# Performance work log

Hardware: AMD Instinct MI355X
Metric: run time of the kernel (lower is better)

Reference implementation:

```python
import jax, jax.numpy as jnp
import numpy as np

N = 100000
E = 1600000
IN_FEATS = 128
HID = 128


def _xavier(key, shape):
    fan_in, fan_out = shape[0], shape[1]
    limit = float(np.sqrt(6.0 / (fan_in + fan_out)))
    return jax.random.uniform(key, shape, jnp.float32, -limit, limit)


def setup_inputs() -> dict:
    key = jax.random.key(0)
    ks = jax.random.split(key, 10)
    x = jax.random.normal(ks[0], (N, IN_FEATS), jnp.float32)
    edge_index = jax.random.randint(ks[1], (2, E), 0, N, jnp.int64)
    inp = {"x": x, "edge_index": edge_index}
    # GCNConv weights (stored as [in, out] so h = x @ W)
    inp["W1"] = _xavier(ks[2], (IN_FEATS, HID)); inp["b1"] = jnp.zeros((HID,), jnp.float32)
    inp["W2"] = _xavier(ks[3], (HID, HID));      inp["b2"] = jnp.zeros((HID,), jnp.float32)
    inp["W3"] = _xavier(ks[4], (HID, HID));      inp["b3"] = jnp.zeros((HID,), jnp.float32)
    # position head: Linear(HID,HID) -> ReLU -> Linear(HID,2)
    inp["Wp1"] = _xavier(ks[5], (HID, HID)); inp["bp1"] = jnp.zeros((HID,), jnp.float32)
    inp["Wp2"] = _xavier(ks[6], (HID, 2));   inp["bp2"] = jnp.zeros((2,), jnp.float32)
    # time head: Linear(HID,HID//2) -> ReLU -> Linear(HID//2,1)
    inp["Wt1"] = _xavier(ks[7], (HID, HID // 2)); inp["bt1"] = jnp.zeros((HID // 2,), jnp.float32)
    inp["Wt2"] = _xavier(ks[8], (HID // 2, 1));   inp["bt2"] = jnp.zeros((1,), jnp.float32)
    return inp


def _gcn_conv(x, src, dst, norm, W, b):
    # PyG GCNConv: out = D^{-1/2} (A + I) D^{-1/2} (x W) + b
    h = x @ W                                  # [N, out]
    msg = h[src] * norm[:, None]               # gather over edges (+ self-loops)
    agg = jax.ops.segment_sum(msg, dst, num_segments=N)  # scatter-add to dst
    return agg + b


def reference(x, edge_index, W1, b1, W2, b2, W3, b3, Wp1, bp1, Wp2, bp2, Wt1, bt1, Wt2, bt2):
    src, dst = edge_index[0], edge_index[1]
    # add self-loops once (shared across the 3 conv layers)
    loop = jnp.arange(N, dtype=edge_index.dtype)
    src_a = jnp.concatenate([src, loop])
    dst_a = jnp.concatenate([dst, loop])
    # symmetric normalization: deg computed on dst (in-degree incl. self-loop)
    deg = jax.ops.segment_sum(jnp.ones_like(dst_a, dtype=x.dtype), dst_a, num_segments=N)
    dinv = jnp.where(deg > 0, jax.lax.rsqrt(deg), 0.0)
    norm = dinv[src_a] * dinv[dst_a]           # [E + N]

    h = jax.nn.relu(_gcn_conv(x, src_a, dst_a, norm, W1, b1))
    h = jax.nn.relu(_gcn_conv(h, src_a, dst_a, norm, W2, b2))
    h = jax.nn.relu(_gcn_conv(h, src_a, dst_a, norm, W3, b3))

    pos = jax.nn.relu(h @ Wp1 + bp1) @ Wp2 + bp2     # [N, 2]
    time = jax.nn.relu(h @ Wt1 + bt1) @ Wt2 + bt2    # [N, 1]
    return jnp.concatenate([pos, time], axis=1)      # [N, 3]
```

## Files before the change

### kernel.cpp

```cpp
#include <hip/hip_runtime.h>

typedef __bf16 bf16x8 __attribute__((ext_vector_type(8)));
typedef unsigned short u16x8 __attribute__((ext_vector_type(8)));
typedef float f32x4 __attribute__((ext_vector_type(4)));

union BU {
    u16x8 u;
    bf16x8 b;
};

static __device__ __forceinline__ float b2f(unsigned short u) {
    return __uint_as_float(((unsigned)u) << 16);
}
static __device__ __forceinline__ unsigned short f2b(float f) {
    unsigned u = __float_as_uint(f);
    unsigned r = (u + 0x7FFF + ((u >> 16) & 1)) >> 16;
    return (unsigned short)r;
}

__global__ __launch_bounds__(256) void wsplit_kernel(
    const float* __restrict__ W1, const float* __restrict__ W2, const float* __restrict__ W3,
    const float* __restrict__ Wp1, const float* __restrict__ Wt1,
    unsigned short* __restrict__ W1hi, unsigned short* __restrict__ W1lo,
    unsigned short* __restrict__ W2hi, unsigned short* __restrict__ W2lo,
    unsigned short* __restrict__ W3hi, unsigned short* __restrict__ W3lo,
    unsigned short* __restrict__ Wchi, unsigned short* __restrict__ Wclo,
    const float* __restrict__ bp1, const float* __restrict__ bt1, float* __restrict__ bcat) {
    int b = blockIdx.x;
    int tid = threadIdx.x;
    if (b < 288) {
        const float* W;
        unsigned short *Whi, *Wlo;
        int lb, ncshift, total;
        if (b < 64)       { W = W1;  Whi = W1hi; Wlo = W1lo; lb = b;       ncshift = 7; total = 16384; }
        else if (b < 128) { W = W2;  Whi = W2hi; Wlo = W2lo; lb = b - 64;  ncshift = 7; total = 16384; }
        else if (b < 192) { W = W3;  Whi = W3hi; Wlo = W3lo; lb = b - 128; ncshift = 7; total = 16384; }
        else if (b < 256) { W = Wp1; Whi = Wchi; Wlo = Wclo; lb = b - 192; ncshift = 7; total = 16384; }
        else              { W = Wt1; Whi = Wchi + 128 * 128; Wlo = Wclo + 128 * 128; lb = b - 256; ncshift = 6; total = 8192; }
        int idx = lb * 256 + tid;
        if (idx < total) {
            int k = idx >> ncshift;
            int n = idx - (k << ncshift);
            float a = W[idx];
            unsigned short hb = f2b(a);
            Whi[(n << 7) + k] = hb;
            Wlo[(n << 7) + k] = f2b(a - b2f(hb));
        }
        return;
    }
    if (tid < 128) bcat[tid] = bp1[tid];
    else if (tid < 192) bcat[tid] = bt1[tid - 128];
}

static __device__ __forceinline__ void split8(const float4 a01, const float4 a23,
                                              bf16x8& hi, bf16x8& lo) {
    float a[8] = {a01.x, a01.y, a01.z, a01.w, a23.x, a23.y, a23.z, a23.w};
    BU h, l;
#pragma unroll
    for (int j = 0; j < 8; ++j) {
        unsigned short hb = f2b(a[j]);
        h.u[j] = hb;
        l.u[j] = f2b(a[j] - b2f(hb));
    }
    hi = h.b;
    lo = l.b;
}

template <int NT>
static __device__ __forceinline__ void gemm_acc_f32(const float* __restrict__ A,
                                                    const unsigned short* __restrict__ Whi,
                                                    const unsigned short* __restrict__ Wlo,
                                                    int arow, int m16, int quad, f32x4* acc) {
    const float* Arow = A + (size_t)arow * 128 + quad * 8;
#pragma unroll
    for (int kb = 0; kb < 4; ++kb) {
        float4 a01 = *reinterpret_cast<const float4*>(Arow + kb * 32);
        float4 a23 = *reinterpret_cast<const float4*>(Arow + kb * 32 + 4);
        bf16x8 ahi, alo;
        split8(a01, a23, ahi, alo);
#pragma unroll
        for (int t = 0; t < NT; ++t) {
            size_t woff = (size_t)(t * 16 + m16) * 128 + quad * 8 + kb * 32;
            BU bh, bl;
            bh.u = *reinterpret_cast<const u16x8*>(Whi + woff);
            bl.u = *reinterpret_cast<const u16x8*>(Wlo + woff);
            acc[t] = __builtin_amdgcn_mfma_f32_16x16x32_bf16(ahi, bh.b, acc[t], 0, 0, 0);
            acc[t] = __builtin_amdgcn_mfma_f32_16x16x32_bf16(ahi, bl.b, acc[t], 0, 0, 0);
            acc[t] = __builtin_amdgcn_mfma_f32_16x16x32_bf16(alo, bh.b, acc[t], 0, 0, 0);
        }
    }
}

template <int NT>
static __device__ __forceinline__ void gemm_acc(const unsigned short* __restrict__ A,
                                                const unsigned short* __restrict__ Whi,
                                                const unsigned short* __restrict__ Wlo,
                                                int arow, int m16, int quad, f32x4* acc) {
    const unsigned short* Arow = A + (size_t)arow * 128 + quad * 8;
#pragma unroll
    for (int kb = 0; kb < 4; ++kb) {
        BU a;
        a.u = *reinterpret_cast<const u16x8*>(Arow + kb * 32);
#pragma unroll
        for (int t = 0; t < NT; ++t) {
            size_t woff = (size_t)(t * 16 + m16) * 128 + quad * 8 + kb * 32;
            BU bh, bl;
            bh.u = *reinterpret_cast<const u16x8*>(Whi + woff);
            bl.u = *reinterpret_cast<const u16x8*>(Wlo + woff);
            acc[t] = __builtin_amdgcn_mfma_f32_16x16x32_bf16(a.b, bh.b, acc[t], 0, 0, 0);
            acc[t] = __builtin_amdgcn_mfma_f32_16x16x32_bf16(a.b, bl.b, acc[t], 0, 0, 0);
        }
    }
}

template <int NT>
static __device__ __forceinline__ void gemm_store_plain(unsigned short* __restrict__ C,
                                                        int row_base, int m16, int quad,
                                                        f32x4* acc, int nrows) {
#pragma unroll
    for (int t = 0; t < NT; ++t) {
#pragma unroll
        for (int r = 0; r < 4; ++r) {
            int row = row_base + quad * 4 + r;
            if (row < nrows)
                C[(size_t)row * (NT * 16) + t * 16 + m16] = f2b(acc[t][r]);
        }
    }
}

template <int NT>
static __device__ __forceinline__ void gemm_store_scaled(const int* __restrict__ deg,
                                                         unsigned short* __restrict__ C,
                                                         int row_base, int m16, int quad,
                                                         f32x4* acc, int nrows) {
#pragma unroll
    for (int t = 0; t < NT; ++t) {
#pragma unroll
        for (int r = 0; r < 4; ++r) {
            int row = row_base + quad * 4 + r;
            if (row < nrows) {
                float d = rsqrtf((float)deg[row] + 1.0f);
                C[(size_t)row * (NT * 16) + t * 16 + m16] = f2b(acc[t][r] * d);
            }
        }
    }
}

__global__ __launch_bounds__(256) void fg2_kernel(const float* __restrict__ A,
                                                  const unsigned short* __restrict__ Whi,
                                                  const unsigned short* __restrict__ Wlo,
                                                  unsigned short* __restrict__ C, int nrows,
                                                  int fbn,
                                                  const int* __restrict__ ei,
                                                  int* __restrict__ deg,
                                                  int* __restrict__ slots, int E) {
    const int bid = blockIdx.x;
    const int tid = threadIdx.x;
    const int trip = bid / 3, r = bid % 3;
    if (r == 1 && trip < fbn) {
        int base = (trip * 256 + tid) * 8;
        int dsts[8], srcs[8], ps[8];
#pragma unroll
        for (int k = 0; k < 8; ++k) {
            int e = base + k;
            dsts[k] = (e < E) ? ei[E + e] : -1;
            srcs[k] = (e < E) ? ei[e] : 0;
        }
#pragma unroll
        for (int k = 0; k < 8; ++k)
            if (dsts[k] >= 0) ps[k] = atomicAdd(&deg[dsts[k]], 1);
#pragma unroll
        for (int k = 0; k < 8; ++k)
            if (dsts[k] >= 0 && ps[k] < 64)
                __builtin_nontemporal_store(srcs[k], &slots[(size_t)dsts[k] * 64 + ps[k]]);
    } else {
        int gid = bid - min(trip, fbn) - ((r > 1 && trip < fbn) ? 1 : 0);
        const int wave = tid >> 6, lane = tid & 63;
        const int m16 = lane & 15, quad = lane >> 4;
        const int row_base = gid * 64 + wave * 16;
        int arow = row_base + m16;
        if (arow >= nrows) arow = nrows - 1;
        f32x4 acc[8] = {};
        gemm_acc_f32<8>(A, Whi, Wlo, arow, m16, quad, acc);
        gemm_store_plain<8>(C, row_base, m16, quad, acc, nrows);
    }
}

__global__ __launch_bounds__(256) void scale_kernel(unsigned short* __restrict__ hs,
                                                    const int* __restrict__ deg, int n) {
    int idx = blockIdx.x * 256 + threadIdx.x;
    int node = idx >> 5;
    if (node >= n) return;
    int f = (idx & 31) * 4;
    float d = rsqrtf((float)deg[node] + 1.0f);
    ushort4 v = *reinterpret_cast<const ushort4*>(hs + (size_t)node * 128 + f);
    ushort4 o;
    o.x = f2b(b2f(v.x) * d);
    o.y = f2b(b2f(v.y) * d);
    o.z = f2b(b2f(v.z) * d);
    o.w = f2b(b2f(v.w) * d);
    *reinterpret_cast<ushort4*>(hs + (size_t)node * 128 + f) = o;
}

template <int NT>
__global__ __launch_bounds__(256) void gemm_kernel(const unsigned short* __restrict__ A,
                                                   const unsigned short* __restrict__ Whi,
                                                   const unsigned short* __restrict__ Wlo,
                                                   const int* __restrict__ deg,
                                                   unsigned short* __restrict__ C, int nrows) {
    const int tid = threadIdx.x;
    const int wave = tid >> 6, lane = tid & 63;
    const int m16 = lane & 15, quad = lane >> 4;
    const int row_base = blockIdx.x * 64 + wave * 16;
    int arow = row_base + m16;
    if (arow >= nrows) arow = nrows - 1;
    f32x4 acc[NT] = {};
    gemm_acc<NT>(A, Whi, Wlo, arow, m16, quad, acc);
    gemm_store_scaled<NT>(deg, C, row_base, m16, quad, acc, nrows);
}

__global__ __launch_bounds__(256) void pull_kernel(const unsigned short* __restrict__ hs,
                                                   const int* __restrict__ slots,
                                                   const int* __restrict__ deg,
                                                   const float* __restrict__ bias,
                                                   unsigned short* __restrict__ out, int n) {
    const int tid = threadIdx.x;
    const int wave = tid >> 6, lane = tid & 63;
    const int slot = lane >> 4, chunk = lane & 15;
    const int node = blockIdx.x * 4 + wave;
    if (node >= n) return;
    const int dg = deg[node];
    const float d = rsqrtf((float)dg + 1.0f);
    const int m = min(dg, 64);

    BU sv;
    sv.u = *reinterpret_cast<const u16x8*>(hs + (size_t)node * 128 + chunk * 8);
    int myidx = slots[(size_t)node * 64 + lane];

    float acc[8] = {};
    const int rounds = (m + 3) >> 2;
    int r = 0;
    for (; r + 4 <= rounds; r += 4) {
        int e0 = r * 4 + slot, e1 = e0 + 4, e2 = e0 + 8, e3 = e0 + 12;
        int s0 = __shfl(myidx, e0), s1 = __shfl(myidx, e1);
        int s2 = __shfl(myidx, e2), s3 = __shfl(myidx, e3);
        s0 = (unsigned)s0 < (unsigned)n ? s0 : 0;
        s1 = (unsigned)s1 < (unsigned)n ? s1 : 0;
        s2 = (unsigned)s2 < (unsigned)n ? s2 : 0;
        s3 = (unsigned)s3 < (unsigned)n ? s3 : 0;
        bool ok0 = e0 < m, ok1 = e1 < m, ok2 = e2 < m, ok3 = e3 < m;
        BU h0, h1, h2, h3;
        if (ok0) h0.u = *reinterpret_cast<const u16x8*>(hs + (size_t)s0 * 128 + chunk * 8);
        if (ok1) h1.u = *reinterpret_cast<const u16x8*>(hs + (size_t)s1 * 128 + chunk * 8);
        if (ok2) h2.u = *reinterpret_cast<const u16x8*>(hs + (size_t)s2 * 128 + chunk * 8);
        if (ok3) h3.u = *reinterpret_cast<const u16x8*>(hs + (size_t)s3 * 128 + chunk * 8);
        if (ok0) {
#pragma unroll
            for (int j = 0; j < 8; ++j) acc[j] += b2f(h0.u[j]);
        }
        if (ok1) {
#pragma unroll
            for (int j = 0; j < 8; ++j) acc[j] += b2f(h1.u[j]);
        }
        if (ok2) {
#pragma unroll
            for (int j = 0; j < 8; ++j) acc[j] += b2f(h2.u[j]);
        }
        if (ok3) {
#pragma unroll
            for (int j = 0; j < 8; ++j) acc[j] += b2f(h3.u[j]);
        }
    }
    for (; r < rounds; ++r) {
        int e0 = r * 4 + slot;
        int s0 = __shfl(myidx, e0);
        s0 = (unsigned)s0 < (unsigned)n ? s0 : 0;
        if (e0 < m) {
            BU h0;
            h0.u = *reinterpret_cast<const u16x8*>(hs + (size_t)s0 * 128 + chunk * 8);
#pragma unroll
            for (int j = 0; j < 8; ++j) acc[j] += b2f(h0.u[j]);
        }
    }
#pragma unroll
    for (int j = 0; j < 8; ++j) {
        acc[j] += __shfl_xor(acc[j], 16);
        acc[j] += __shfl_xor(acc[j], 32);
    }
    if (slot == 0) {
        BU o;
#pragma unroll
        for (int j = 0; j < 8; ++j)
            o.u[j] = f2b(fmaxf((acc[j] + b2f(sv.u[j])) * d + bias[chunk * 8 + j], 0.f));
        *reinterpret_cast<u16x8*>(out + (size_t)node * 128 + chunk * 8) = o.u;
    }
}

__global__ __launch_bounds__(256) void gemmh_kernel(const unsigned short* __restrict__ A,
                                                    const unsigned short* __restrict__ Whi,
                                                    const unsigned short* __restrict__ Wlo,
                                                    const float* __restrict__ bcat,
                                                    const float* __restrict__ Wp2,
                                                    const float* __restrict__ bp2,
                                                    const float* __restrict__ Wt2,
                                                    const float* __restrict__ bt2,
                                                    float* __restrict__ out, int nrows) {
    const int tid = threadIdx.x;
    const int wave = tid >> 6, lane = tid & 63;
    const int m16 = lane & 15, quad = lane >> 4;
    const int row_base = blockIdx.x * 64 + wave * 16;
    int arow = row_base + m16;
    if (arow >= nrows) arow = nrows - 1;
    f32x4 acc[12] = {};
    gemm_acc<12>(A, Whi, Wlo, arow, m16, quad, acc);
#pragma unroll
    for (int r = 0; r < 4; ++r) {
        int row = row_base + quad * 4 + r;
        float p0 = 0.f, p1 = 0.f, tt = 0.f;
#pragma unroll
        for (int t = 0; t < 12; ++t) {
            int c = t * 16 + m16;
            float v = fmaxf(acc[t][r] + bcat[c], 0.f);
            if (t < 8) {
                p0 += v * Wp2[c * 2 + 0];
                p1 += v * Wp2[c * 2 + 1];
            } else {
                tt += v * Wt2[c - 128];
            }
        }
#pragma unroll
        for (int mask = 1; mask < 16; mask <<= 1) {
            p0 += __shfl_xor(p0, mask);
            p1 += __shfl_xor(p1, mask);
            tt += __shfl_xor(tt, mask);
        }
        if (m16 == 0 && row < nrows) {
            out[(size_t)row * 3 + 0] = p0 + bp2[0];
            out[(size_t)row * 3 + 1] = p1 + bp2[1];
            out[(size_t)row * 3 + 2] = tt + bt2[0];
        }
    }
}

extern "C" void kernel_launch(void* const* d_in, const int* in_sizes, int n_in,
                              void* d_out, int out_size, void* d_ws, size_t ws_size,
                              hipStream_t stream) {
    const int N = in_sizes[0] / 128;
    const int E = in_sizes[1] / 2;

    const float* x   = (const float*)d_in[0];
    const int* ei    = (const int*)d_in[1];
    const float* W1  = (const float*)d_in[2];
    const float* b1  = (const float*)d_in[3];
    const float* W2  = (const float*)d_in[4];
    const float* b2  = (const float*)d_in[5];
    const float* W3  = (const float*)d_in[6];
    const float* b3  = (const float*)d_in[7];
    const float* Wp1 = (const float*)d_in[8];
    const float* bp1 = (const float*)d_in[9];
    const float* Wp2 = (const float*)d_in[10];
    const float* bp2 = (const float*)d_in[11];
    const float* Wt1 = (const float*)d_in[12];
    const float* bt1 = (const float*)d_in[13];
    const float* Wt2 = (const float*)d_in[14];
    const float* bt2 = (const float*)d_in[15];
    float* out = (float*)d_out;

    char* ws = (char*)d_ws;
    size_t off = 0;
    auto alloc = [&](size_t bytes) {
        void* p = ws + off;
        off += (bytes + 255) & ~(size_t)255;
        return p;
    };
    int* deg        = (int*)alloc((size_t)N * 4);
    int* slots      = (int*)alloc((size_t)N * 64 * 4);
    unsigned short* W1hi = (unsigned short*)alloc(16384 * 2);
    unsigned short* W1lo = (unsigned short*)alloc(16384 * 2);
    unsigned short* W2hi = (unsigned short*)alloc(16384 * 2);
    unsigned short* W2lo = (unsigned short*)alloc(16384 * 2);
    unsigned short* W3hi = (unsigned short*)alloc(16384 * 2);
    unsigned short* W3lo = (unsigned short*)alloc(16384 * 2);
    unsigned short* Wchi = (unsigned short*)alloc(192 * 128 * 2);
    unsigned short* Wclo = (unsigned short*)alloc(192 * 128 * 2);
    float* bcat          = (float*)alloc(192 * 4);
    unsigned short* hs   = (unsigned short*)alloc((size_t)N * 128 * 2);
    unsigned short* hb   = (unsigned short*)alloc((size_t)N * 128 * 2);

    hipMemsetAsync(deg, 0, (size_t)N * 4, stream);

    wsplit_kernel<<<289, 256, 0, stream>>>(W1, W2, W3, Wp1, Wt1,
                                           W1hi, W1lo, W2hi, W2lo, W3hi, W3lo,
                                           Wchi, Wclo, bp1, bt1, bcat);

    const int gb = (N + 63) / 64;
    const int fbn = ((E + 7) / 8 + 255) / 256;
    const int pull_blocks = (N + 3) / 4;

    fg2_kernel<<<gb + fbn, 256, 0, stream>>>(x, W1hi, W1lo, hs, N, fbn, ei, deg, slots, E);
    scale_kernel<<<(N * 32 + 255) / 256, 256, 0, stream>>>(hs, deg, N);

    pull_kernel<<<pull_blocks, 256, 0, stream>>>(hs, slots, deg, b1, hb, N);
    gemm_kernel<8><<<gb, 256, 0, stream>>>(hb, W2hi, W2lo, deg, hs, N);
    pull_kernel<<<pull_blocks, 256, 0, stream>>>(hs, slots, deg, b2, hb, N);
    gemm_kernel<8><<<gb, 256, 0, stream>>>(hb, W3hi, W3lo, deg, hs, N);
    pull_kernel<<<pull_blocks, 256, 0, stream>>>(hs, slots, deg, b3, hb, N);

    gemmh_kernel<<<gb, 256, 0, stream>>>(hb, Wchi, Wclo, bcat, Wp2, bp2, Wt2, bt2, out, N);
}
```

Before: 631.9 us.

## Fuse neighbor aggregation with following GEMM through LDS staging

Merges each pull (gather-aggregate) kernel with the next layer's GEMM (or the output heads GEMM). Each wave aggregates 16 nodes sequentially into a padded LDS tile and then runs the MFMA GEMM from LDS. This removes the round trip of the intermediate bf16 activation buffer through global memory and several kernel launches. In exchange, each wave now walks its 16 nodes one after another, so there is less parallelism and fewer blocks in flight for latency hiding during the gather.

```diff
diff --git a/kernel.cpp b/kernel.cpp
--- a/kernel.cpp
+++ b/kernel.cpp
@@ -17,6 +17,8 @@
     unsigned r = (u + 0x7FFF + ((u >> 16) & 1)) >> 16;
     return (unsigned short)r;
 }
+
+#define LROW 136
 
 __global__ __launch_bounds__(256) void wsplit_kernel(
     const float* __restrict__ W1, const float* __restrict__ W2, const float* __restrict__ W3,
@@ -92,11 +94,11 @@
 }
 
 template <int NT>
-static __device__ __forceinline__ void gemm_acc(const unsigned short* __restrict__ A,
-                                                const unsigned short* __restrict__ Whi,
-                                                const unsigned short* __restrict__ Wlo,
-                                                int arow, int m16, int quad, f32x4* acc) {
-    const unsigned short* Arow = A + (size_t)arow * 128 + quad * 8;
+static __device__ __forceinline__ void gemm_acc_lds(const unsigned short* __restrict__ Alds,
+                                                    const unsigned short* __restrict__ Whi,
+                                                    const unsigned short* __restrict__ Wlo,
+                                                    int m16, int quad, f32x4* acc) {
+    const unsigned short* Arow = Alds + m16 * LROW + quad * 8;
 #pragma unroll
     for (int kb = 0; kb < 4; ++kb) {
         BU a;
@@ -202,37 +204,12 @@
     *reinterpret_cast<ushort4*>(hs + (size_t)node * 128 + f) = o;
 }
 
-template <int NT>
-__global__ __launch_bounds__(256) void gemm_kernel(const unsigned short* __restrict__ A,
-                                                   const unsigned short* __restrict__ Whi,
-                                                   const unsigned short* __restrict__ Wlo,
-                                                   const int* __restrict__ deg,
-                                                   unsigned short* __restrict__ C, int nrows) {
-    const int tid = threadIdx.x;
-    const int wave = tid >> 6, lane = tid & 63;
-    const int m16 = lane & 15, quad = lane >> 4;
-    const int row_base = blockIdx.x * 64 + wave * 16;
-    int arow = row_base + m16;
-    if (arow >= nrows) arow = nrows - 1;
-    f32x4 acc[NT] = {};
-    gemm_acc<NT>(A, Whi, Wlo, arow, m16, quad, acc);
-    gemm_store_scaled<NT>(deg, C, row_base, m16, quad, acc, nrows);
-}
-
-__global__ __launch_bounds__(256) void pull_kernel(const unsigned short* __restrict__ hs,
-                                                   const int* __restrict__ slots,
-                                                   const int* __restrict__ deg,
-                                                   const float* __restrict__ bias,
-                                                   unsigned short* __restrict__ out, int n) {
-    const int tid = threadIdx.x;
-    const int wave = tid >> 6, lane = tid & 63;
-    const int slot = lane >> 4, chunk = lane & 15;
-    const int node = blockIdx.x * 4 + wave;
-    if (node >= n) return;
-    const int dg = deg[node];
-    const float d = rsqrtf((float)dg + 1.0f);
+static __device__ __forceinline__ void pull_node(const unsigned short* __restrict__ hs,
+                                                 const int* __restrict__ slots,
+                                                 int node, int dg, float d, const float* bi,
+                                                 unsigned short* __restrict__ ldsrow,
+                                                 int slot, int chunk, int lane, int n) {
     const int m = min(dg, 64);
-
     BU sv;
     sv.u = *reinterpret_cast<const u16x8*>(hs + (size_t)node * 128 + chunk * 8);
     int myidx = slots[(size_t)node * 64 + lane];
@@ -291,28 +268,83 @@
         BU o;
 #pragma unroll
         for (int j = 0; j < 8; ++j)
-            o.u[j] = f2b(fmaxf((acc[j] + b2f(sv.u[j])) * d + bias[chunk * 8 + j], 0.f));
-        *reinterpret_cast<u16x8*>(out + (size_t)node * 128 + chunk * 8) = o.u;
-    }
-}
-
-__global__ __launch_bounds__(256) void gemmh_kernel(const unsigned short* __restrict__ A,
-                                                    const unsigned short* __restrict__ Whi,
-                                                    const unsigned short* __restrict__ Wlo,
-                                                    const float* __restrict__ bcat,
-                                                    const float* __restrict__ Wp2,
-                                                    const float* __restrict__ bp2,
-                                                    const float* __restrict__ Wt2,
-                                                    const float* __restrict__ bt2,
-                                                    float* __restrict__ out, int nrows) {
+            o.u[j] = f2b(fmaxf((acc[j] + b2f(sv.u[j])) * d + bi[j], 0.f));
+        *reinterpret_cast<u16x8*>(ldsrow + chunk * 8) = o.u;
+    }
+}
+
+__global__ __launch_bounds__(256) void pg_kernel(const unsigned short* __restrict__ hs_in,
+                                                 const int* __restrict__ slots,
+                                                 const int* __restrict__ deg,
+                                                 const float* __restrict__ bias,
+                                                 const unsigned short* __restrict__ Whi,
+                                                 const unsigned short* __restrict__ Wlo,
+                                                 unsigned short* __restrict__ hs_out, int n) {
+    __shared__ unsigned short lds[4 * 16 * LROW];
     const int tid = threadIdx.x;
     const int wave = tid >> 6, lane = tid & 63;
+    const int slot = lane >> 4, chunk = lane & 15;
+    const int row_base = blockIdx.x * 64 + wave * 16;
+    unsigned short* wl = lds + wave * 16 * LROW;
+
+    float bi[8];
+#pragma unroll
+    for (int j = 0; j < 8; ++j) bi[j] = bias[chunk * 8 + j];
+
+    for (int i = 0; i < 16; ++i) {
+        int node = row_base + i;
+        if (node < n) {
+            int dg = deg[node];
+            float d = rsqrtf((float)dg + 1.0f);
+            pull_node(hs_in, slots, node, dg, d, bi, wl + i * LROW, slot, chunk, lane, n);
+        } else if (slot == 0) {
+            u16x8 z = {};
+            *reinterpret_cast<u16x8*>(wl + i * LROW + chunk * 8) = z;
+        }
+    }
     const int m16 = lane & 15, quad = lane >> 4;
+    f32x4 acc[8] = {};
+    gemm_acc_lds<8>(wl, Whi, Wlo, m16, quad, acc);
+    gemm_store_scaled<8>(deg, hs_out, row_base, m16, quad, acc, n);
+}
+
+__global__ __launch_bounds__(256) void pgh_kernel(const unsigned short* __restrict__ hs_in,
+                                                  const int* __restrict__ slots,
+                                                  const int* __restrict__ deg,
+                                                  const float* __restrict__ bias,
+                                                  const unsigned short* __restrict__ Whi,
+                                                  const unsigned short* __restrict__ Wlo,
+                                                  const float* __restrict__ bcat,
+                                                  const float* __restrict__ Wp2,
+                                                  const float* __restrict__ bp2,
+                                                  const float* __restrict__ Wt2,
+                                                  const float* __restrict__ bt2,
+                                                  float* __restrict__ out, int n) {
+    __shared__ unsigned short lds[4 * 16 * LROW];
+    const int tid = threadIdx.x;
+    const int wave = tid >> 6, lane = tid & 63;
+    const int slot = lane >> 4, chunk = lane & 15;
     const int row_base = blockIdx.x * 64 + wave * 16;
-    int arow = row_base + m16;
-    if (arow >= nrows) arow = nrows - 1;
+    unsigned short* wl = lds + wave * 16 * LROW;
+
+    float bi[8];
+#pragma unroll
+    for (int j = 0; j < 8; ++j) bi[j] = bias[chunk * 8 + j];
+
+    for (int i = 0; i < 16; ++i) {
+        int node = row_base + i;
+        if (node < n) {
+            int dg = deg[node];
+            float d = rsqrtf((float)dg + 1.0f);
+            pull_node(hs_in, slots, node, dg, d, bi, wl + i * LROW, slot, chunk, lane, n);
+        } else if (slot == 0) {
+            u16x8 z = {};
+            *reinterpret_cast<u16x8*>(wl + i * LROW + chunk * 8) = z;
+        }
+    }
+    const int m16 = lane & 15, quad = lane >> 4;
     f32x4 acc[12] = {};
-    gemm_acc<12>(A, Whi, Wlo, arow, m16, quad, acc);
+    gemm_acc_lds<12>(wl, Whi, Wlo, m16, quad, acc);
 #pragma unroll
     for (int r = 0; r < 4; ++r) {
         int row = row_base + quad * 4 + r;
@@ -334,7 +366,7 @@
             p1 += __shfl_xor(p1, mask);
             tt += __shfl_xor(tt, mask);
         }
-        if (m16 == 0 && row < nrows) {
+        if (m16 == 0 && row < n) {
             out[(size_t)row * 3 + 0] = p0 + bp2[0];
             out[(size_t)row * 3 + 1] = p1 + bp2[1];
             out[(size_t)row * 3 + 2] = tt + bt2[0];
@@ -384,8 +416,8 @@
     unsigned short* Wchi = (unsigned short*)alloc(192 * 128 * 2);
     unsigned short* Wclo = (unsigned short*)alloc(192 * 128 * 2);
     float* bcat          = (float*)alloc(192 * 4);
-    unsigned short* hs   = (unsigned short*)alloc((size_t)N * 128 * 2);
-    unsigned short* hb   = (unsigned short*)alloc((size_t)N * 128 * 2);
+    unsigned short* hsA  = (unsigned short*)alloc((size_t)N * 128 * 2);
+    unsigned short* hsB  = (unsigned short*)alloc((size_t)N * 128 * 2);
 
     hipMemsetAsync(deg, 0, (size_t)N * 4, stream);
 
@@ -395,16 +427,12 @@
 
     const int gb = (N + 63) / 64;
     const int fbn = ((E + 7) / 8 + 255) / 256;
-    const int pull_blocks = (N + 3) / 4;
-
-    fg2_kernel<<<gb + fbn, 256, 0, stream>>>(x, W1hi, W1lo, hs, N, fbn, ei, deg, slots, E);
-    scale_kernel<<<(N * 32 + 255) / 256, 256, 0, stream>>>(hs, deg, N);
-
-    pull_kernel<<<pull_blocks, 256, 0, stream>>>(hs, slots, deg, b1, hb, N);
-    gemm_kernel<8><<<gb, 256, 0, stream>>>(hb, W2hi, W2lo, deg, hs, N);
-    pull_kernel<<<pull_blocks, 256, 0, stream>>>(hs, slots, deg, b2, hb, N);
-    gemm_kernel<8><<<gb, 256, 0, stream>>>(hb, W3hi, W3lo, deg, hs, N);
-    pull_kernel<<<pull_blocks, 256, 0, stream>>>(hs, slots, deg, b3, hb, N);
-
-    gemmh_kernel<<<gb, 256, 0, stream>>>(hb, Wchi, Wclo, bcat, Wp2, bp2, Wt2, bt2, out, N);
-}
+
+    fg2_kernel<<<gb + fbn, 256, 0, stream>>>(x, W1hi, W1lo, hsA, N, fbn, ei, deg, slots, E);
+    scale_kernel<<<(N * 32 + 255) / 256, 256, 0, stream>>>(hsA, deg, N);
+
+    pg_kernel<<<gb, 256, 0, stream>>>(hsA, slots, deg, b1, W2hi, W2lo, hsB, N);
+    pg_kernel<<<gb, 256, 0, stream>>>(hsB, slots, deg, b2, W3hi, W3lo, hsA, N);
+    pgh_kernel<<<gb, 256, 0, stream>>>(hsA, slots, deg, b3, Wchi, Wclo, bcat,
+                                       Wp2, bp2, Wt2, bt2, out, N);
+}
```

Result: slower. 673.7 us (+6.6%).

## Store node features in 16-column feature slices for cache-local neighbor gathers

Applied to the files above, without the earlier changes.

Node feature buffers move from row-major [N,128] to eight feature slices of [N,16]. The pull kernel now handles one slice per block, so each node's gathered working set is 3.2 MB per slice, which may stay cache-resident across neighbors. Each wave now covers up to 64 neighbors with one 16-byte load per lane, where before it looped in rounds. The GEMM, scale and head kernels are updated for the sliced layout. In exchange, the pull kernel launches eight times as many blocks, re-reads slot lists and degrees once per slice, and needs more shuffle reductions.

```diff
diff --git a/kernel.cpp b/kernel.cpp
--- a/kernel.cpp
+++ b/kernel.cpp
@@ -17,6 +17,7 @@
     unsigned r = (u + 0x7FFF + ((u >> 16) & 1)) >> 16;
     return (unsigned short)r;
 }
+
 
 __global__ __launch_bounds__(256) void wsplit_kernel(
     const float* __restrict__ W1, const float* __restrict__ W2, const float* __restrict__ W3,
@@ -92,18 +93,19 @@
 }
 
 template <int NT>
-static __device__ __forceinline__ void gemm_acc(const unsigned short* __restrict__ A,
-                                                const unsigned short* __restrict__ Whi,
-                                                const unsigned short* __restrict__ Wlo,
-                                                int arow, int m16, int quad, f32x4* acc) {
-    const unsigned short* Arow = A + (size_t)arow * 128 + quad * 8;
+static __device__ __forceinline__ void gemm_acc_sliced(const unsigned short* __restrict__ A,
+                                                       const unsigned short* __restrict__ Whi,
+                                                       const unsigned short* __restrict__ Wlo,
+                                                       int arow, int m16, int quad, f32x4* acc,
+                                                       int Nn) {
 #pragma unroll
     for (int kb = 0; kb < 4; ++kb) {
+        int f0 = kb * 32 + quad * 8;
         BU a;
-        a.u = *reinterpret_cast<const u16x8*>(Arow + kb * 32);
+        a.u = *reinterpret_cast<const u16x8*>(A + ((size_t)(f0 >> 4) * Nn + arow) * 16 + (f0 & 15));
 #pragma unroll
         for (int t = 0; t < NT; ++t) {
-            size_t woff = (size_t)(t * 16 + m16) * 128 + quad * 8 + kb * 32;
+            size_t woff = (size_t)(t * 16 + m16) * 128 + f0;
             BU bh, bl;
             bh.u = *reinterpret_cast<const u16x8*>(Whi + woff);
             bl.u = *reinterpret_cast<const u16x8*>(Wlo + woff);
@@ -114,25 +116,25 @@
 }
 
 template <int NT>
-static __device__ __forceinline__ void gemm_store_plain(unsigned short* __restrict__ C,
-                                                        int row_base, int m16, int quad,
-                                                        f32x4* acc, int nrows) {
+static __device__ __forceinline__ void gemm_store_plain_sliced(unsigned short* __restrict__ C,
+                                                               int row_base, int m16, int quad,
+                                                               f32x4* acc, int nrows) {
 #pragma unroll
     for (int t = 0; t < NT; ++t) {
 #pragma unroll
         for (int r = 0; r < 4; ++r) {
             int row = row_base + quad * 4 + r;
             if (row < nrows)
-                C[(size_t)row * (NT * 16) + t * 16 + m16] = f2b(acc[t][r]);
-        }
-    }
-}
-
-template <int NT>
-static __device__ __forceinline__ void gemm_store_scaled(const int* __restrict__ deg,
-                                                         unsigned short* __restrict__ C,
-                                                         int row_base, int m16, int quad,
-                                                         f32x4* acc, int nrows) {
+                C[((size_t)t * nrows + row) * 16 + m16] = f2b(acc[t][r]);
+        }
+    }
+}
+
+template <int NT>
+static __device__ __forceinline__ void gemm_store_scaled_sliced(const int* __restrict__ deg,
+                                                                unsigned short* __restrict__ C,
+                                                                int row_base, int m16, int quad,
+                                                                f32x4* acc, int nrows) {
 #pragma unroll
     for (int t = 0; t < NT; ++t) {
 #pragma unroll
@@ -140,7 +142,7 @@
             int row = row_base + quad * 4 + r;
             if (row < nrows) {
                 float d = rsqrtf((float)deg[row] + 1.0f);
-                C[(size_t)row * (NT * 16) + t * 16 + m16] = f2b(acc[t][r] * d);
+                C[((size_t)t * nrows + row) * 16 + m16] = f2b(acc[t][r] * d);
             }
         }
     }
@@ -182,24 +184,24 @@
         if (arow >= nrows) arow = nrows - 1;
         f32x4 acc[8] = {};
         gemm_acc_f32<8>(A, Whi, Wlo, arow, m16, quad, acc);
-        gemm_store_plain<8>(C, row_base, m16, quad, acc, nrows);
+        gemm_store_plain_sliced<8>(C, row_base, m16, quad, acc, nrows);
     }
 }
 
 __global__ __launch_bounds__(256) void scale_kernel(unsigned short* __restrict__ hs,
                                                     const int* __restrict__ deg, int n) {
-    int idx = blockIdx.x * 256 + threadIdx.x;
-    int node = idx >> 5;
+    int i = blockIdx.x * 256 + threadIdx.x;
+    int node = i >> 1;
     if (node >= n) return;
-    int f = (idx & 31) * 4;
+    int half = i & 1;
+    unsigned short* p = hs + ((size_t)blockIdx.y * n + node) * 16 + half * 8;
     float d = rsqrtf((float)deg[node] + 1.0f);
-    ushort4 v = *reinterpret_cast<const ushort4*>(hs + (size_t)node * 128 + f);
-    ushort4 o;
-    o.x = f2b(b2f(v.x) * d);
-    o.y = f2b(b2f(v.y) * d);
-    o.z = f2b(b2f(v.z) * d);
-    o.w = f2b(b2f(v.w) * d);
-    *reinterpret_cast<ushort4*>(hs + (size_t)node * 128 + f) = o;
+    BU v;
+    v.u = *reinterpret_cast<const u16x8*>(p);
+    BU o;
+#pragma unroll
+    for (int j = 0; j < 8; ++j) o.u[j] = f2b(b2f(v.u[j]) * d);
+    *reinterpret_cast<u16x8*>(p) = o.u;
 }
 
 template <int NT>
@@ -215,8 +217,8 @@
     int arow = row_base + m16;
     if (arow >= nrows) arow = nrows - 1;
     f32x4 acc[NT] = {};
-    gemm_acc<NT>(A, Whi, Wlo, arow, m16, quad, acc);
-    gemm_store_scaled<NT>(deg, C, row_base, m16, quad, acc, nrows);
+    gemm_acc_sliced<NT>(A, Whi, Wlo, arow, m16, quad, acc, nrows);
+    gemm_store_scaled_sliced<NT>(deg, C, row_base, m16, quad, acc, nrows);
 }
 
 __global__ __launch_bounds__(256) void pull_kernel(const unsigned short* __restrict__ hs,
@@ -226,64 +228,42 @@
                                                    unsigned short* __restrict__ out, int n) {
     const int tid = threadIdx.x;
     const int wave = tid >> 6, lane = tid & 63;
-    const int slot = lane >> 4, chunk = lane & 15;
-    const int node = blockIdx.x * 4 + wave;
+    const int slot = lane >> 1, half = lane & 1;
+    const int slice = blockIdx.x & 7;
+    const int node = (blockIdx.x >> 3) * 4 + wave;
     if (node >= n) return;
     const int dg = deg[node];
+    const int m = min(dg, 64);
     const float d = rsqrtf((float)dg + 1.0f);
-    const int m = min(dg, 64);
+    const unsigned short* base = hs + (size_t)slice * n * 16 + half * 8;
 
     BU sv;
-    sv.u = *reinterpret_cast<const u16x8*>(hs + (size_t)node * 128 + chunk * 8);
-    int myidx = slots[(size_t)node * 64 + lane];
-
+    sv.u = *reinterpret_cast<const u16x8*>(base + (size_t)node * 16);
+    int myidx = __builtin_nontemporal_load(&slots[(size_t)node * 64 + lane]);
+
+    int e0 = slot, e1 = 32 + slot;
+    int s0 = __shfl(myidx, e0);
+    int s1 = __shfl(myidx, e1);
+    s0 = (unsigned)s0 < (unsigned)n ? s0 : 0;
+    s1 = (unsigned)s1 < (unsigned)n ? s1 : 0;
+    bool ok0 = e0 < m, ok1 = e1 < m;
+    BU h0, h1;
+    if (ok0) h0.u = *reinterpret_cast<const u16x8*>(base + (size_t)s0 * 16);
+    if (ok1) h1.u = *reinterpret_cast<const u16x8*>(base + (size_t)s1 * 16);
     float acc[8] = {};
-    const int rounds = (m + 3) >> 2;
-    int r = 0;
-    for (; r + 4 <= rounds; r += 4) {
-        int e0 = r * 4 + slot, e1 = e0 + 4, e2 = e0 + 8, e3 = e0 + 12;
-        int s0 = __shfl(myidx, e0), s1 = __shfl(myidx, e1);
-        int s2 = __shfl(myidx, e2), s3 = __shfl(myidx, e3);
-        s0 = (unsigned)s0 < (unsigned)n ? s0 : 0;
-        s1 = (unsigned)s1 < (unsigned)n ? s1 : 0;
-        s2 = (unsigned)s2 < (unsigned)n ? s2 : 0;
-        s3 = (unsigned)s3 < (unsigned)n ? s3 : 0;
-        bool ok0 = e0 < m, ok1 = e1 < m, ok2 = e2 < m, ok3 = e3 < m;
-        BU h0, h1, h2, h3;
-        if (ok0) h0.u = *reinterpret_cast<const u16x8*>(hs + (size_t)s0 * 128 + chunk * 8);
-        if (ok1) h1.u = *reinterpret_cast<const u16x8*>(hs + (size_t)s1 * 128 + chunk * 8);
-        if (ok2) h2.u = *reinterpret_cast<const u16x8*>(hs + (size_t)s2 * 128 + chunk * 8);
-        if (ok3) h3.u = *reinterpret_cast<const u16x8*>(hs + (size_t)s3 * 128 + chunk * 8);
-        if (ok0) {
-#pragma unroll
-            for (int j = 0; j < 8; ++j) acc[j] += b2f(h0.u[j]);
-        }
-        if (ok1) {
-#pragma unroll
-            for (int j = 0; j < 8; ++j) acc[j] += b2f(h1.u[j]);
-        }
-        if (ok2) {
-#pragma unroll
-            for (int j = 0; j < 8; ++j) acc[j] += b2f(h2.u[j]);
-        }
-        if (ok3) {
-#pragma unroll
-            for (int j = 0; j < 8; ++j) acc[j] += b2f(h3.u[j]);
-        }
-    }
-    for (; r < rounds; ++r) {
-        int e0 = r * 4 + slot;
-        int s0 = __shfl(myidx, e0);
-        s0 = (unsigned)s0 < (unsigned)n ? s0 : 0;
-        if (e0 < m) {
-            BU h0;
-            h0.u = *reinterpret_cast<const u16x8*>(hs + (size_t)s0 * 128 + chunk * 8);
-#pragma unroll
-            for (int j = 0; j < 8; ++j) acc[j] += b2f(h0.u[j]);
-        }
+    if (ok0) {
+#pragma unroll
+        for (int j = 0; j < 8; ++j) acc[j] += b2f(h0.u[j]);
+    }
+    if (ok1) {
+#pragma unroll
+        for (int j = 0; j < 8; ++j) acc[j] += b2f(h1.u[j]);
     }
 #pragma unroll
     for (int j = 0; j < 8; ++j) {
+        acc[j] += __shfl_xor(acc[j], 2);
+        acc[j] += __shfl_xor(acc[j], 4);
+        acc[j] += __shfl_xor(acc[j], 8);
         acc[j] += __shfl_xor(acc[j], 16);
         acc[j] += __shfl_xor(acc[j], 32);
     }
@@ -291,8 +271,8 @@
         BU o;
 #pragma unroll
         for (int j = 0; j < 8; ++j)
-            o.u[j] = f2b(fmaxf((acc[j] + b2f(sv.u[j])) * d + bias[chunk * 8 + j], 0.f));
-        *reinterpret_cast<u16x8*>(out + (size_t)node * 128 + chunk * 8) = o.u;
+            o.u[j] = f2b(fmaxf((acc[j] + b2f(sv.u[j])) * d + bias[slice * 16 + half * 8 + j], 0.f));
+        *reinterpret_cast<u16x8*>(out + ((size_t)slice * n + node) * 16 + half * 8) = o.u;
     }
 }
 
@@ -312,7 +292,7 @@
     int arow = row_base + m16;
     if (arow >= nrows) arow = nrows - 1;
     f32x4 acc[12] = {};
-    gemm_acc<12>(A, Whi, Wlo, arow, m16, quad, acc);
+    gemm_acc_sliced<12>(A, Whi, Wlo, arow, m16, quad, acc, nrows);
 #pragma unroll
     for (int r = 0; r < 4; ++r) {
         int row = row_base + quad * 4 + r;
@@ -384,8 +364,8 @@
     unsigned short* Wchi = (unsigned short*)alloc(192 * 128 * 2);
     unsigned short* Wclo = (unsigned short*)alloc(192 * 128 * 2);
     float* bcat          = (float*)alloc(192 * 4);
-    unsigned short* hs   = (unsigned short*)alloc((size_t)N * 128 * 2);
-    unsigned short* hb   = (unsigned short*)alloc((size_t)N * 128 * 2);
+    unsigned short* hsA  = (unsigned short*)alloc((size_t)N * 128 * 2);
+    unsigned short* hsB  = (unsigned short*)alloc((size_t)N * 128 * 2);
 
     hipMemsetAsync(deg, 0, (size_t)N * 4, stream);
 
@@ -395,16 +375,16 @@
 
     const int gb = (N + 63) / 64;
     const int fbn = ((E + 7) / 8 + 255) / 256;
-    const int pull_blocks = (N + 3) / 4;
-
-    fg2_kernel<<<gb + fbn, 256, 0, stream>>>(x, W1hi, W1lo, hs, N, fbn, ei, deg, slots, E);
-    scale_kernel<<<(N * 32 + 255) / 256, 256, 0, stream>>>(hs, deg, N);
-
-    pull_kernel<<<pull_blocks, 256, 0, stream>>>(hs, slots, deg, b1, hb, N);
-    gemm_kernel<8><<<gb, 256, 0, stream>>>(hb, W2hi, W2lo, deg, hs, N);
-    pull_kernel<<<pull_blocks, 256, 0, stream>>>(hs, slots, deg, b2, hb, N);
-    gemm_kernel<8><<<gb, 256, 0, stream>>>(hb, W3hi, W3lo, deg, hs, N);
-    pull_kernel<<<pull_blocks, 256, 0, stream>>>(hs, slots, deg, b3, hb, N);
-
-    gemmh_kernel<<<gb, 256, 0, stream>>>(hb, Wchi, Wclo, bcat, Wp2, bp2, Wt2, bt2, out, N);
-}
+    const int pull_blocks = 8 * ((N + 3) / 4);
+
+    fg2_kernel<<<gb + fbn, 256, 0, stream>>>(x, W1hi, W1lo, hsA, N, fbn, ei, deg, slots, E);
+    scale_kernel<<<dim3((N * 2 + 255) / 256, 8), 256, 0, stream>>>(hsA, deg, N);
+
+    pull_kernel<<<pull_blocks, 256, 0, stream>>>(hsA, slots, deg, b1, hsB, N);
+    gemm_kernel<8><<<gb, 256, 0, stream>>>(hsB, W2hi, W2lo, deg, hsA, N);
+    pull_kernel<<<pull_blocks, 256, 0, stream>>>(hsA, slots, deg, b2, hsB, N);
+    gemm_kernel<8><<<gb, 256, 0, stream>>>(hsB, W3hi, W3lo, deg, hsA, N);
+    pull_kernel<<<pull_blocks, 256, 0, stream>>>(hsA, slots, deg, b3, hsB, N);
+
+    gemmh_kernel<<<gb, 256, 0, stream>>>(hsB, Wchi, Wclo, bcat, Wp2, bp2, Wt2, bt2, out, N);
+}
```

After: 1.483 ms. 135% more time.

## Overlap next-layer GEMM with remaining pull aggregation via split mixed kernels

Applied to the files above, without the earlier changes.

Splits each pull (aggregation) stage into a first part covering nodes [0,C0) and a remainder. A combined kernel runs the next layer's GEMM on the finished rows alongside the remaining pull blocks, then a tail GEMM finishes the rows past C0. The aim is to run the compute-bound GEMM concurrently with the memory-bound gather and cut idle tails between launches. It adds a third activation buffer and more launches, and relies on the GEMM blocks only reading rows the earlier pull already finished.

```diff
diff --git a/kernel.cpp b/kernel.cpp
--- a/kernel.cpp
+++ b/kernel.cpp
@@ -146,89 +146,33 @@
     }
 }
 
-__global__ __launch_bounds__(256) void fg2_kernel(const float* __restrict__ A,
-                                                  const unsigned short* __restrict__ Whi,
-                                                  const unsigned short* __restrict__ Wlo,
-                                                  unsigned short* __restrict__ C, int nrows,
-                                                  int fbn,
-                                                  const int* __restrict__ ei,
-                                                  int* __restrict__ deg,
-                                                  int* __restrict__ slots, int E) {
-    const int bid = blockIdx.x;
-    const int tid = threadIdx.x;
-    const int trip = bid / 3, r = bid % 3;
-    if (r == 1 && trip < fbn) {
-        int base = (trip * 256 + tid) * 8;
-        int dsts[8], srcs[8], ps[8];
-#pragma unroll
-        for (int k = 0; k < 8; ++k) {
-            int e = base + k;
-            dsts[k] = (e < E) ? ei[E + e] : -1;
-            srcs[k] = (e < E) ? ei[e] : 0;
-        }
-#pragma unroll
-        for (int k = 0; k < 8; ++k)
-            if (dsts[k] >= 0) ps[k] = atomicAdd(&deg[dsts[k]], 1);
-#pragma unroll
-        for (int k = 0; k < 8; ++k)
-            if (dsts[k] >= 0 && ps[k] < 64)
-                __builtin_nontemporal_store(srcs[k], &slots[(size_t)dsts[k] * 64 + ps[k]]);
-    } else {
-        int gid = bid - min(trip, fbn) - ((r > 1 && trip < fbn) ? 1 : 0);
-        const int wave = tid >> 6, lane = tid & 63;
-        const int m16 = lane & 15, quad = lane >> 4;
-        const int row_base = gid * 64 + wave * 16;
-        int arow = row_base + m16;
-        if (arow >= nrows) arow = nrows - 1;
-        f32x4 acc[8] = {};
-        gemm_acc_f32<8>(A, Whi, Wlo, arow, m16, quad, acc);
-        gemm_store_plain<8>(C, row_base, m16, quad, acc, nrows);
-    }
-}
-
-__global__ __launch_bounds__(256) void scale_kernel(unsigned short* __restrict__ hs,
-                                                    const int* __restrict__ deg, int n) {
-    int idx = blockIdx.x * 256 + threadIdx.x;
-    int node = idx >> 5;
-    if (node >= n) return;
-    int f = (idx & 31) * 4;
-    float d = rsqrtf((float)deg[node] + 1.0f);
-    ushort4 v = *reinterpret_cast<const ushort4*>(hs + (size_t)node * 128 + f);
-    ushort4 o;
-    o.x = f2b(b2f(v.x) * d);
-    o.y = f2b(b2f(v.y) * d);
-    o.z = f2b(b2f(v.z) * d);
-    o.w = f2b(b2f(v.w) * d);
-    *reinterpret_cast<ushort4*>(hs + (size_t)node * 128 + f) = o;
-}
-
-template <int NT>
-__global__ __launch_bounds__(256) void gemm_kernel(const unsigned short* __restrict__ A,
-                                                   const unsigned short* __restrict__ Whi,
-                                                   const unsigned short* __restrict__ Wlo,
-                                                   const int* __restrict__ deg,
-                                                   unsigned short* __restrict__ C, int nrows) {
-    const int tid = threadIdx.x;
+static __device__ __forceinline__ void gemm_body(int gid, int tid, int row0,
+                                                 const unsigned short* __restrict__ A,
+                                                 const unsigned short* __restrict__ Whi,
+                                                 const unsigned short* __restrict__ Wlo,
+                                                 const int* __restrict__ deg,
+                                                 unsigned short* __restrict__ C, int nrows) {
     const int wave = tid >> 6, lane = tid & 63;
     const int m16 = lane & 15, quad = lane >> 4;
-    const int row_base = blockIdx.x * 64 + wave * 16;
+    const int row_base = row0 + gid * 64 + wave * 16;
     int arow = row_base + m16;
     if (arow >= nrows) arow = nrows - 1;
-    f32x4 acc[NT] = {};
-    gemm_acc<NT>(A, Whi, Wlo, arow, m16, quad, acc);
-    gemm_store_scaled<NT>(deg, C, row_base, m16, quad, acc, nrows);
-}
-
-__global__ __launch_bounds__(256) void pull_kernel(const unsigned short* __restrict__ hs,
-                                                   const int* __restrict__ slots,
-                                                   const int* __restrict__ deg,
-                                                   const float* __restrict__ bias,
-                                                   unsigned short* __restrict__ out, int n) {
-    const int tid = threadIdx.x;
+    f32x4 acc[8] = {};
+    gemm_acc<8>(A, Whi, Wlo, arow, m16, quad, acc);
+    gemm_store_scaled<8>(deg, C, row_base, m16, quad, acc, nrows);
+}
+
+static __device__ __forceinline__ void pull_body(int bid, int tid,
+                                                 const unsigned short* __restrict__ hs,
+                                                 const int* __restrict__ slots,
+                                                 const int* __restrict__ deg,
+                                                 const float* __restrict__ bias,
+                                                 unsigned short* __restrict__ out,
+                                                 int node0, int node1, int n) {
     const int wave = tid >> 6, lane = tid & 63;
     const int slot = lane >> 4, chunk = lane & 15;
-    const int node = blockIdx.x * 4 + wave;
-    if (node >= n) return;
+    const int node = node0 + bid * 4 + wave;
+    if (node >= node1) return;
     const int dg = deg[node];
     const float d = rsqrtf((float)dg + 1.0f);
     const int m = min(dg, 64);
@@ -296,19 +240,19 @@
     }
 }
 
-__global__ __launch_bounds__(256) void gemmh_kernel(const unsigned short* __restrict__ A,
-                                                    const unsigned short* __restrict__ Whi,
-                                                    const unsigned short* __restrict__ Wlo,
-                                                    const float* __restrict__ bcat,
-                                                    const float* __restrict__ Wp2,
-                                                    const float* __restrict__ bp2,
-                                                    const float* __restrict__ Wt2,
-                                                    const float* __restrict__ bt2,
-                                                    float* __restrict__ out, int nrows) {
-    const int tid = threadIdx.x;
+static __device__ __forceinline__ void heads_body(int gid, int tid, int row0,
+                                                  const unsigned short* __restrict__ A,
+                                                  const unsigned short* __restrict__ Whi,
+                                                  const unsigned short* __restrict__ Wlo,
+                                                  const float* __restrict__ bcat,
+                                                  const float* __restrict__ Wp2,
+                                                  const float* __restrict__ bp2,
+                                                  const float* __restrict__ Wt2,
+                                                  const float* __restrict__ bt2,
+                                                  float* __restrict__ out, int nrows) {
     const int wave = tid >> 6, lane = tid & 63;
     const int m16 = lane & 15, quad = lane >> 4;
-    const int row_base = blockIdx.x * 64 + wave * 16;
+    const int row_base = row0 + gid * 64 + wave * 16;
     int arow = row_base + m16;
     if (arow >= nrows) arow = nrows - 1;
     f32x4 acc[12] = {};
@@ -339,6 +283,136 @@
             out[(size_t)row * 3 + 1] = p1 + bp2[1];
             out[(size_t)row * 3 + 2] = tt + bt2[0];
         }
+    }
+}
+
+__global__ __launch_bounds__(256) void fg2_kernel(const float* __restrict__ A,
+                                                  const unsigned short* __restrict__ Whi,
+                                                  const unsigned short* __restrict__ Wlo,
+                                                  unsigned short* __restrict__ C, int nrows,
+                                                  int fbn,
+                                                  const int* __restrict__ ei,
+                                                  int* __restrict__ deg,
+                                                  int* __restrict__ slots, int E) {
+    const int bid = blockIdx.x;
+    const int tid = threadIdx.x;
+    const int trip = bid / 3, r = bid % 3;
+    if (r == 1 && trip < fbn) {
+        int base = (trip * 256 + tid) * 8;
+        int dsts[8], srcs[8], ps[8];
+#pragma unroll
+        for (int k = 0; k < 8; ++k) {
+            int e = base + k;
+            dsts[k] = (e < E) ? ei[E + e] : -1;
+            srcs[k] = (e < E) ? ei[e] : 0;
+        }
+#pragma unroll
+        for (int k = 0; k < 8; ++k)
+            if (dsts[k] >= 0) ps[k] = atomicAdd(&deg[dsts[k]], 1);
+#pragma unroll
+        for (int k = 0; k < 8; ++k)
+            if (dsts[k] >= 0 && ps[k] < 64)
+                __builtin_nontemporal_store(srcs[k], &slots[(size_t)dsts[k] * 64 + ps[k]]);
+    } else {
+        int gid = bid - min(trip, fbn) - ((r > 1 && trip < fbn) ? 1 : 0);
+        const int wave = tid >> 6, lane = tid & 63;
+        const int m16 = lane & 15, quad = lane >> 4;
+        const int row_base = gid * 64 + wave * 16;
+        int arow = row_base + m16;
+        if (arow >= nrows) arow = nrows - 1;
+        f32x4 acc[8] = {};
+        gemm_acc_f32<8>(A, Whi, Wlo, arow, m16, quad, acc);
+        gemm_store_plain<8>(C, row_base, m16, quad, acc, nrows);
+    }
+}
+
+__global__ __launch_bounds__(256) void scale_kernel(unsigned short* __restrict__ hs,
+                                                    const int* __restrict__ deg, int n) {
+    int idx = blockIdx.x * 256 + threadIdx.x;
+    int node = idx >> 5;
+    if (node >= n) return;
+    int f = (idx & 31) * 4;
+    float d = rsqrtf((float)deg[node] + 1.0f);
+    ushort4 v = *reinterpret_cast<const ushort4*>(hs + (size_t)node * 128 + f);
+    ushort4 o;
+    o.x = f2b(b2f(v.x) * d);
+    o.y = f2b(b2f(v.y) * d);
+    o.z = f2b(b2f(v.z) * d);
+    o.w = f2b(b2f(v.w) * d);
+    *reinterpret_cast<ushort4*>(hs + (size_t)node * 128 + f) = o;
+}
+
+__global__ __launch_bounds__(256) void pull_kernel(const unsigned short* __restrict__ hs,
+                                                   const int* __restrict__ slots,
+                                                   const int* __restrict__ deg,
+                                                   const float* __restrict__ bias,
+                                                   unsigned short* __restrict__ out,
+                                                   int node0, int node1, int n) {
+    pull_body(blockIdx.x, threadIdx.x, hs, slots, deg, bias, out, node0, node1, n);
+}
+
+__global__ __launch_bounds__(256) void gemm_kernel(const unsigned short* __restrict__ A,
+                                                   const unsigned short* __restrict__ Whi,
+                                                   const unsigned short* __restrict__ Wlo,
+                                                   const int* __restrict__ deg,
+                                                   unsigned short* __restrict__ C,
+                                                   int row0, int nrows) {
+    gemm_body(blockIdx.x, threadIdx.x, row0, A, Whi, Wlo, deg, C, nrows);
+}
+
+__global__ __launch_bounds__(256) void gemmh_kernel(const unsigned short* __restrict__ A,
+                                                    const unsigned short* __restrict__ Whi,
+                                                    const unsigned short* __restrict__ Wlo,
+                                                    const float* __restrict__ bcat,
+                                                    const float* __restrict__ Wp2,
+                                                    const float* __restrict__ bp2,
+                                                    const float* __restrict__ Wt2,
+                                                    const float* __restrict__ bt2,
+                                                    float* __restrict__ out,
+                                                    int row0, int nrows) {
+    heads_body(blockIdx.x, threadIdx.x, row0, A, Whi, Wlo, bcat, Wp2, bp2, Wt2, bt2, out, nrows);
+}
+
+__global__ __launch_bounds__(256) void mixpg_kernel(const unsigned short* __restrict__ gin,
+                                                    const unsigned short* __restrict__ Whi,
+                                                    const unsigned short* __restrict__ Wlo,
+                                                    const int* __restrict__ deg,
+                                                    unsigned short* __restrict__ gout,
+                                                    const unsigned short* __restrict__ psrc,
+                                                    const int* __restrict__ slots,
+                                                    const float* __restrict__ bias,
+                                                    unsigned short* __restrict__ pout,
+                                                    int gb0, int C0, int n) {
+    const int bid = blockIdx.x;
+    const int tid = threadIdx.x;
+    if (bid < gb0) {
+        gemm_body(bid, tid, 0, gin, Whi, Wlo, deg, gout, n);
+    } else {
+        pull_body(bid - gb0, tid, psrc, slots, deg, bias, pout, C0, n, n);
+    }
+}
+
+__global__ __launch_bounds__(256) void mixph_kernel(const unsigned short* __restrict__ gin,
+                                                    const unsigned short* __restrict__ Whi,
+                                                    const unsigned short* __restrict__ Wlo,
+                                                    const float* __restrict__ bcat,
+                                                    const float* __restrict__ Wp2,
+                                                    const float* __restrict__ bp2,
+                                                    const float* __restrict__ Wt2,
+                                                    const float* __restrict__ bt2,
+                                                    float* __restrict__ out,
+                                                    const int* __restrict__ deg,
+                                                    const unsigned short* __restrict__ psrc,
+                                                    const int* __restrict__ slots,
+                                                    const float* __restrict__ bias,
+                                                    unsigned short* __restrict__ pout,
+                                                    int gb0, int C0, int n) {
+    const int bid = blockIdx.x;
+    const int tid = threadIdx.x;
+    if (bid < gb0) {
+        heads_body(bid, tid, 0, gin, Whi, Wlo, bcat, Wp2, bp2, Wt2, bt2, out, n);
+    } else {
+        pull_body(bid - gb0, tid, psrc, slots, deg, bias, pout, C0, n, n);
     }
 }
 
@@ -384,8 +458,9 @@
     unsigned short* Wchi = (unsigned short*)alloc(192 * 128 * 2);
     unsigned short* Wclo = (unsigned short*)alloc(192 * 128 * 2);
     float* bcat          = (float*)alloc(192 * 4);
-    unsigned short* hs   = (unsigned short*)alloc((size_t)N * 128 * 2);
-    unsigned short* hb   = (unsigned short*)alloc((size_t)N * 128 * 2);
+    unsigned short* hsA  = (unsigned short*)alloc((size_t)N * 128 * 2);
+    unsigned short* hsB  = (unsigned short*)alloc((size_t)N * 128 * 2);
+    unsigned short* hsC  = (unsigned short*)alloc((size_t)N * 128 * 2);
 
     hipMemsetAsync(deg, 0, (size_t)N * 4, stream);
 
@@ -395,16 +470,29 @@
 
     const int gb = (N + 63) / 64;
     const int fbn = ((E + 7) / 8 + 255) / 256;
-    const int pull_blocks = (N + 3) / 4;
-
-    fg2_kernel<<<gb + fbn, 256, 0, stream>>>(x, W1hi, W1lo, hs, N, fbn, ei, deg, slots, E);
-    scale_kernel<<<(N * 32 + 255) / 256, 256, 0, stream>>>(hs, deg, N);
-
-    pull_kernel<<<pull_blocks, 256, 0, stream>>>(hs, slots, deg, b1, hb, N);
-    gemm_kernel<8><<<gb, 256, 0, stream>>>(hb, W2hi, W2lo, deg, hs, N);
-    pull_kernel<<<pull_blocks, 256, 0, stream>>>(hs, slots, deg, b2, hb, N);
-    gemm_kernel<8><<<gb, 256, 0, stream>>>(hb, W3hi, W3lo, deg, hs, N);
-    pull_kernel<<<pull_blocks, 256, 0, stream>>>(hs, slots, deg, b3, hb, N);
-
-    gemmh_kernel<<<gb, 256, 0, stream>>>(hb, Wchi, Wclo, bcat, Wp2, bp2, Wt2, bt2, out, N);
-}
+
+    int C0 = (N * 3 / 4) & ~63;
+    if (C0 < 64) C0 = (N >= 64) ? 64 : 0;
+    const int gb0 = C0 / 64;
+    const int gbr = (N - C0 + 63) / 64;
+    const int pb0 = (C0 + 3) / 4;
+    const int pb1 = (N - C0 + 3) / 4;
+
+    fg2_kernel<<<gb + fbn, 256, 0, stream>>>(x, W1hi, W1lo, hsA, N, fbn, ei, deg, slots, E);
+    scale_kernel<<<(N * 32 + 255) / 256, 256, 0, stream>>>(hsA, deg, N);
+
+    pull_kernel<<<pb0, 256, 0, stream>>>(hsA, slots, deg, b1, hsB, 0, C0, N);
+    mixpg_kernel<<<gb0 + pb1, 256, 0, stream>>>(hsB, W2hi, W2lo, deg, hsC,
+                                                hsA, slots, b1, hsB, gb0, C0, N);
+    gemm_kernel<<<gbr, 256, 0, stream>>>(hsB, W2hi, W2lo, deg, hsC, C0, N);
+
+    pull_kernel<<<pb0, 256, 0, stream>>>(hsC, slots, deg, b2, hsA, 0, C0, N);
+    mixpg_kernel<<<gb0 + pb1, 256, 0, stream>>>(hsA, W3hi, W3lo, deg, hsB,
+                                                hsC, slots, b2, hsA, gb0, C0, N);
+    gemm_kernel<<<gbr, 256, 0, stream>>>(hsA, W3hi, W3lo, deg, hsB, C0, N);
+
+    pull_kernel<<<pb0, 256, 0, stream>>>(hsB, slots, deg, b3, hsC, 0, C0, N);
+    mixph_kernel<<<gb0 + pb1, 256, 0, stream>>>(hsC, Wchi, Wclo, bcat, Wp2, bp2, Wt2, bt2, out,
+                                                deg, hsB, slots, b3, hsC, gb0, C0, N);
+    gemmh_kernel<<<gbr, 256, 0, stream>>>(hsC, Wchi, Wclo, bcat, Wp2, bp2, Wt2, bt2, out, C0, N);
+}
```

New measurement: 653.6 us. 1.03x slower.
